# Optimization experiments

Hardware: AMD Instinct MI355X
Metric: run time of the kernel (lower is better)

Reference implementation:

```python
import jax, jax.numpy as jnp
import numpy as np

K = 8
NUM_BLOCKS = 4
ALPHA = K / (K + 1)  # 8/9


def _knn_norm_adj(xyz, k):
    """xyz: (B, 3, N) -> symmetric-normalized GCN adjacency (B, N, N).

    Mirrors knn_point(k, xyz, xyz) -> indices[:, 1:] -> get_adjacency_matrix,
    then the (input-independent) DenseGCNConv normalization: self loops set to 1,
    deg clamped >= 1, D^-1/2 A D^-1/2. adj is identical for every GCN call, so
    it is normalized once here.
    """
    x2 = jnp.sum(xyz * xyz, axis=1)                       # (B, N)
    inner = jnp.einsum('bci,bcj->bij', xyz, xyz)          # (B, N, N)
    dist = x2[:, :, None] + x2[:, None, :] - 2.0 * inner  # squared pairwise dist
    _, idx = jax.lax.top_k(-dist, k)                      # (B, N, k); self (dist 0) first
    nbr = idx[:, :, 1:]                                   # drop self -> k-1 neighbors
    B, N = x2.shape
    adj = jnp.zeros((B, N, N), xyz.dtype)
    adj = adj.at[jnp.arange(B)[:, None, None],
                 jnp.arange(N)[None, :, None], nbr].set(1.0)
    ar = jnp.arange(N)
    adj = adj.at[:, ar, ar].set(1.0)                      # add_loop=True
    dis = jnp.clip(jnp.sum(adj, axis=-1), 1.0, None) ** -0.5  # (B, N)
    return dis[:, :, None] * adj * dis[:, None, :]


def setup_inputs() -> dict:
    key = jax.random.key(0)
    ks = jax.random.split(key, 6)
    B, N, C = 16, 2048, 128
    s = 1.0 / np.sqrt(C).astype(np.float32)
    return {
        'xyz': jax.random.normal(ks[0], (B, 3, N), jnp.float32),
        'points': jax.random.normal(ks[1], (B, C, N), jnp.float32),
        'Wc': jax.random.normal(ks[2], (4, C, C), jnp.float32) * s,   # nn.Linear weights (out,in)
        'Wg': jax.random.normal(ks[3], (4, C, C), jnp.float32) * s,   # DenseGCNConv lin weights
        'Wuc': jax.random.normal(ks[4], (6, C), jnp.float32) * s,
        'Wug': jax.random.normal(ks[5], (6, C), jnp.float32) * s,
    }


def reference(xyz, points, Wc, Wg, Wuc, Wug):
    adj = _knn_norm_adj(xyz, K)                 # (B, N, N)
    pts = jnp.swapaxes(points, 1, 2)            # (B, N, C) channel-last internally
    for i in range(NUM_BLOCKS):
        shortcut = pts
        act = jax.nn.relu(pts)
        center = jnp.einsum('bnc,dc->bnd', act, Wc[i])                 # Linear on relu(points)
        grouped = adj @ jnp.einsum('bnc,dc->bnd', shortcut, Wg[i])     # DenseGCNConv on shortcut
        pts = (1.0 - ALPHA) * grouped + ALPHA * center + shortcut
    # unpool head
    points_xyz = jnp.einsum('bnd,od->bno', pts, Wuc)                   # (B, N, 6)
    grouped_xyz = adj @ jnp.einsum('bnd,od->bno', pts, Wug)            # (B, N, 6)
    new = ALPHA * points_xyz + (1.0 - ALPHA) * grouped_xyz
    B, N, _ = new.shape
    new = jnp.swapaxes(new, 1, 2).reshape(B, 3, 2, N) + xyz[:, :, None, :]
    new_xyz = new.reshape(B, 3, 2 * N)
    return new_xyz, jnp.swapaxes(pts, 1, 2)     # ((B,3,2N), (B,C,N))
```

## Files before the change

kernel.cpp:

```cpp
#include <hip/hip_runtime.h>
#include <hip/hip_bf16.h>

static constexpr int NB = 16;
static constexpr int NP = 2048;
static constexpr int NC = 128;
#define ALPHA_F ((float)(8.0/9.0))
#define OMA_F   ((float)(1.0 - 8.0/9.0))

typedef __attribute__((ext_vector_type(8))) short bfrag;
typedef __attribute__((ext_vector_type(4))) float ffrag;

union BU { bfrag v; uint4 u; unsigned int w[4]; };

__device__ inline void split2(float x, float y, unsigned& hi, unsigned& lo) {
    __hip_bfloat162 h = __float22bfloat162_rn(make_float2(x, y));
    float2 hb = __bfloat1622float2(h);
    __hip_bfloat162 l = __float22bfloat162_rn(make_float2(x - hb.x, y - hb.y));
    __builtin_memcpy(&hi, &h, 4);
    __builtin_memcpy(&lo, &l, 4);
}

__device__ inline void split1(float x, unsigned short& h, unsigned short& l) {
    __hip_bfloat16 hb = __float2bfloat16(x);
    float hf = __bfloat162float(hb);
    __hip_bfloat16 lb = __float2bfloat16(x - hf);
    __builtin_memcpy(&h, &hb, 2);
    __builtin_memcpy(&l, &lb, 2);
}

__global__ __launch_bounds__(256) void knn_kernel(const float* __restrict__ xyz,
                                                  int* __restrict__ nbr) {
    __shared__ float4 sp[NP];
    __shared__ float  md[64][33];
    __shared__ int    mi[64][33];
    int b = blockIdx.y;
    const float* X = xyz + (size_t)b * 3 * NP;
    for (int m = threadIdx.x; m < NP; m += 256) {
        float x = X[m], y = X[NP + m], z = X[2 * NP + m];
        sp[m ^ ((m >> 5) & 7)] = make_float4(x, y, z, x * x + y * y + z * z);
    }
    __syncthreads();

    int tid = threadIdx.x;
    int p = tid >> 2;
    int q = tid & 3;
    int base = blockIdx.x * 64;
    int n = base + p;
    float4 me = sp[n ^ ((n >> 5) & 7)];
    float xi = me.x, yi = me.y, zi = me.z, qi = me.w;

    unsigned gd[8];
#pragma unroll
    for (int t = 0; t < 8; ++t) gd[t] = 0x7F7FFFFFu;
#pragma unroll 1
    for (int gg = 0; gg < 16; ++gg) {
        int g = q * 16 + gg;
        const float4* gp = sp + g * 32;
        float m0 = 3.4e38f, m1 = m0, m2 = m0, m3 = m0;
#pragma unroll
        for (int k = 0; k < 32; k += 4) {
            float4 a0 = gp[(k + 0) ^ q];
            float4 a1 = gp[(k + 1) ^ q];
            float4 a2 = gp[(k + 2) ^ q];
            float4 a3 = gp[(k + 3) ^ q];
            m0 = fminf(m0, qi + a0.w - 2.0f * (xi * a0.x + yi * a0.y + zi * a0.z));
            m1 = fminf(m1, qi + a1.w - 2.0f * (xi * a1.x + yi * a1.y + zi * a1.z));
            m2 = fminf(m2, qi + a2.w - 2.0f * (xi * a2.x + yi * a2.y + zi * a2.z));
            m3 = fminf(m3, qi + a3.w - 2.0f * (xi * a3.x + yi * a3.y + zi * a3.z));
        }
        float gm = fmaxf(fminf(fminf(m0, m1), fminf(m2, m3)), 0.0f);
        unsigned pg; __builtin_memcpy(&pg, &gm, 4);
        pg = (pg & ~63u) | (unsigned)g;
        unsigned prev = gd[0];
        gd[0] = gd[0] < pg ? gd[0] : pg;
#pragma unroll
        for (int t = 1; t < 8; ++t) {
            unsigned mx = prev > pg ? prev : pg;
            prev = gd[t];
            gd[t] = gd[t] < mx ? gd[t] : mx;
        }
    }

#define CEU(A, B) { unsigned _lo = (A) < (B) ? (A) : (B); \
                    unsigned _hi = (A) < (B) ? (B) : (A); (A) = _lo; (B) = _hi; }
    unsigned cA[8];
#pragma unroll
    for (int i = 0; i < 8; ++i) {
        unsigned pb = (unsigned)__shfl_xor((int)gd[7 - i], 1);
        cA[i] = gd[i] < pb ? gd[i] : pb;
    }
    CEU(cA[0], cA[4]); CEU(cA[1], cA[5]); CEU(cA[2], cA[6]); CEU(cA[3], cA[7]);
    CEU(cA[0], cA[2]); CEU(cA[1], cA[3]); CEU(cA[4], cA[6]); CEU(cA[5], cA[7]);
    CEU(cA[0], cA[1]); CEU(cA[2], cA[3]); CEU(cA[4], cA[5]); CEU(cA[6], cA[7]);
    unsigned dA[8];
#pragma unroll
    for (int i = 0; i < 8; ++i) {
        unsigned pb = (unsigned)__shfl_xor((int)cA[7 - i], 2);
        dA[i] = cA[i] < pb ? cA[i] : pb;
    }
    unsigned long long mask = 0ull;
#pragma unroll
    for (int i = 0; i < 8; ++i) mask |= (1ull << (dA[i] & 63u));

    float bd[8]; int bi[8];
#pragma unroll
    for (int t = 0; t < 8; ++t) { bd[t] = 3.4e38f; bi[t] = 0; }
    while (mask) {
        int g = (int)__builtin_ctzll(mask);
        mask &= (mask - 1ull);
        int sw = g & 7;
        int jb = g * 32 + q;
#pragma unroll
        for (int i = 0; i < 8; ++i) {
            int j0 = jb + i * 4;
            float4 c4v = sp[j0 ^ sw];
            float inner = xi * c4v.x + yi * c4v.y + zi * c4v.z;
            float d = qi + c4v.w - 2.0f * inner;
            bool c[8];
#pragma unroll
            for (int t = 0; t < 8; ++t) c[t] = d < bd[t];
#pragma unroll
            for (int t = 7; t >= 1; --t) {
                bd[t] = c[t - 1] ? bd[t - 1] : (c[t] ? d : bd[t]);
                bi[t] = c[t - 1] ? bi[t - 1] : (c[t] ? j0 : bi[t]);
            }
            bd[0] = c[0] ? d : bd[0];
            bi[0] = c[0] ? j0 : bi[0];
        }
    }
#pragma unroll
    for (int t = 0; t < 8; ++t) {
        md[p][q * 8 + t] = bd[t];
        mi[p][q * 8 + t] = bi[t];
    }
    __syncthreads();

    if (tid < 64) {
        float fd[8]; int fi[8];
#pragma unroll
        for (int t = 0; t < 8; ++t) { fd[t] = 3.4e38f; fi[t] = 0; }
#pragma unroll 4
        for (int cc = 0; cc < 32; ++cc) {
            float d = md[tid][cc];
            int j = mi[tid][cc];
            bool c[8];
#pragma unroll
            for (int t = 0; t < 8; ++t) c[t] = d < fd[t];
#pragma unroll
            for (int t = 7; t >= 1; --t) {
                fd[t] = c[t - 1] ? fd[t - 1] : (c[t] ? d : fd[t]);
                fi[t] = c[t - 1] ? fi[t - 1] : (c[t] ? j : fi[t]);
            }
            fd[0] = c[0] ? d : fd[0];
            fi[0] = c[0] ? j : fi[0];
        }
        int row = b * NP + base + tid;
#pragma unroll
        for (int t = 0; t < 7; ++t) nbr[row * 7 + t] = fi[t + 1];
    }
}

__global__ __launch_bounds__(256) void transpose_kernel(const float* __restrict__ in,
                                                        float* __restrict__ out,
                                                        int R, int S) {
    __shared__ float t[32][33];
    int b = blockIdx.z;
    int s0 = blockIdx.x * 32, r0 = blockIdx.y * 32;
    const float* I = in + (size_t)b * R * S;
    float* O = out + (size_t)b * R * S;
#pragma unroll
    for (int i = 0; i < 4; ++i) {
        int r = r0 + threadIdx.y + i * 8;
        t[threadIdx.y + i * 8][threadIdx.x] = I[(size_t)r * S + s0 + threadIdx.x];
    }
    __syncthreads();
#pragma unroll
    for (int i = 0; i < 4; ++i) {
        int s = s0 + threadIdx.y + i * 8;
        O[(size_t)s * R + r0 + threadIdx.x] = t[threadIdx.x][threadIdx.y + i * 8];
    }
}

__global__ __launch_bounds__(256) void prep_w_kernel(const float* __restrict__ Wc,
                                                     const float* __restrict__ Wg,
                                                     uint4* __restrict__ WP) {
    int t = blockIdx.x * 256 + threadIdx.x;
    int ncol = t & 127;
    int quad = (t >> 7) & 3;
    int s = (t >> 9) & 3;
    int mat = (t >> 11) & 1;
    int layer = t >> 12;
    const float* W = (mat ? Wg : Wc) + (size_t)layer * NC * NC + (size_t)ncol * NC + s * 32 + quad * 8;
    float4 a = *((const float4*)W);
    float4 b = *((const float4*)(W + 4));
    BU hi, lo;
    split2(a.x, a.y, hi.w[0], lo.w[0]);
    split2(a.z, a.w, hi.w[1], lo.w[1]);
    split2(b.x, b.y, hi.w[2], lo.w[2]);
    split2(b.z, b.w, hi.w[3], lo.w[3]);
    WP[t * 2] = hi.u;
    WP[t * 2 + 1] = lo.u;
}

template <int MODE>
__global__ __launch_bounds__(512) void gemm_fused_kernel(const float* __restrict__ Asrc,
                                                         const float* __restrict__ Y2in,
                                                         const int* __restrict__ nbr,
                                                         const uint4* __restrict__ WPc,
                                                         const uint4* __restrict__ WPg,
                                                         float* __restrict__ Zout,
                                                         float* __restrict__ Y2out) {
    __shared__ unsigned short AhT[64][136];
    __shared__ unsigned short AlT[64][136];
    __shared__ int s_nb[448];
    int tid = threadIdx.x;
    int wid = tid >> 6, lane = tid & 63;
    int quad = lane >> 4, l15 = lane & 15;
    int xcd = blockIdx.x & 7;
    int slot = blockIdx.x >> 3;
    int bb = xcd * 2 + (slot >> 5);
    int n0 = (slot & 31) << 6;
    size_t m0 = (size_t)bb * NP + n0;
    int ncol = wid * 16 + l15;

    BU Bch[4], Bcl[4], Bgh[4], Bgl[4];
#pragma unroll
    for (int s = 0; s < 4; ++s) {
        int idx = ((s * 4 + quad) * 128 + ncol) * 2;
        Bch[s].u = WPc[idx];
        Bcl[s].u = WPc[idx + 1];
        Bgh[s].u = WPg[idx];
        Bgl[s].u = WPg[idx + 1];
    }

    if (MODE == 1) {
        if (tid < 448) s_nb[tid] = nbr[m0 * 7 + tid];
        __syncthreads();
        size_t bbase = (size_t)bb * NP;
#pragma unroll 1
        for (int it = 0; it < 4; ++it) {
            int f = tid + it * 512;
            int r = f >> 5, c4 = (f & 31) * 4;
            size_t row = m0 + r;
            float4 z = *((const float4*)(Asrc + row * NC + c4));
            float4 acc = *((const float4*)(Y2in + row * NC + c4));
#pragma unroll
            for (int t = 0; t < 7; ++t) {
                int j = s_nb[r * 7 + t];
                float4 v = *((const float4*)(Y2in + (bbase + (size_t)j) * NC + c4));
                acc.x += v.x; acc.y += v.y; acc.z += v.z; acc.w += v.w;
            }
            float4 a;
            a.x = OMA_F * (0.125f * acc.x) + z.x;
            a.y = OMA_F * (0.125f * acc.y) + z.y;
            a.z = OMA_F * (0.125f * acc.z) + z.z;
            a.w = OMA_F * (0.125f * acc.w) + z.w;
            unsigned h01, l01, h23, l23;
            split2(a.x, a.y, h01, l01);
            split2(a.z, a.w, h23, l23);
            *((uint2*)&AhT[r][c4]) = make_uint2(h01, h23);
            *((uint2*)&AlT[r][c4]) = make_uint2(l01, l23);
        }
    } else {
#pragma unroll
        for (int it = 0; it < 4; ++it) {
            int f = tid + it * 512;
            int c = f >> 4, rq = (f & 15) * 4;
            float4 v = *((const float4*)(Asrc + ((size_t)bb * NC + c) * NP + n0 + rq));
            float vv[4] = {v.x, v.y, v.z, v.w};
#pragma unroll
            for (int k = 0; k < 4; ++k) {
                unsigned short h, l;
                split1(vv[k], h, l);
                AhT[rq + k][c] = h;
                AlT[rq + k][c] = l;
            }
        }
    }
    __syncthreads();

    ffrag accC[4], accG[4];
#pragma unroll
    for (int mt = 0; mt < 4; ++mt) { accC[mt] = (ffrag)0.0f; accG[mt] = (ffrag)0.0f; }

#pragma unroll
    for (int s = 0; s < 4; ++s) {
#pragma unroll
        for (int mt = 0; mt < 4; ++mt) {
            int m = mt * 16 + l15;
            int k = s * 32 + quad * 8;
            BU ah, al, rh, rl;
            ah.u = *((const uint4*)&AhT[m][k]);
            al.u = *((const uint4*)&AlT[m][k]);
#pragma unroll
            for (int w = 0; w < 4; ++w) {
                unsigned msk = ((ah.w[w] & 0x80008000u) >> 15) * 0xFFFFu;
                rh.w[w] = ah.w[w] & ~msk;
                rl.w[w] = al.w[w] & ~msk;
            }
            accC[mt] = __builtin_amdgcn_mfma_f32_16x16x32_bf16(rh.v, Bch[s].v, accC[mt], 0, 0, 0);
            accC[mt] = __builtin_amdgcn_mfma_f32_16x16x32_bf16(rh.v, Bcl[s].v, accC[mt], 0, 0, 0);
            accC[mt] = __builtin_amdgcn_mfma_f32_16x16x32_bf16(rl.v, Bch[s].v, accC[mt], 0, 0, 0);
            accG[mt] = __builtin_amdgcn_mfma_f32_16x16x32_bf16(ah.v, Bgh[s].v, accG[mt], 0, 0, 0);
            accG[mt] = __builtin_amdgcn_mfma_f32_16x16x32_bf16(ah.v, Bgl[s].v, accG[mt], 0, 0, 0);
            accG[mt] = __builtin_amdgcn_mfma_f32_16x16x32_bf16(al.v, Bgh[s].v, accG[mt], 0, 0, 0);
        }
    }

#pragma unroll
    for (int mt = 0; mt < 4; ++mt) {
        int rbase = mt * 16 + quad * 4;
#pragma unroll
        for (int r = 0; r < 4; ++r) {
            int rr = rbase + r;
            unsigned hb = ((unsigned)AhT[rr][ncol]) << 16;
            unsigned lb = ((unsigned)AlT[rr][ncol]) << 16;
            float hp, lp;
            __builtin_memcpy(&hp, &hb, 4);
            __builtin_memcpy(&lp, &lb, 4);
            float p = hp + lp;
            size_t idx = (m0 + rr) * NC + ncol;
            Zout[idx] = p + ALPHA_F * accC[mt][r];
            Y2out[idx] = accG[mt][r];
        }
    }
}

__global__ __launch_bounds__(256) void agg_kernel(const float* __restrict__ Z,
                                                  const float* __restrict__ Y2,
                                                  const int* __restrict__ nbr,
                                                  float* __restrict__ Pout) {
    int tid = threadIdx.x;
    int lane = tid & 31, rl = tid >> 5;
    int xcd = blockIdx.x & 7;
    int slot = blockIdx.x >> 3;
    int bb = xcd * 2 + (slot >> 8);
    int rblk = slot & 255;
    size_t row = ((size_t)bb << 11) + rblk * 8 + rl;
    const int* nb = nbr + row * 7;
    size_t off = row * NC + lane * 4;
    float4 ys = *((const float4*)(Y2 + off));
    size_t bbase = (size_t)bb * NP * NC;
#pragma unroll
    for (int t = 0; t < 7; ++t) {
        int j = nb[t];
        float4 v = *((const float4*)(Y2 + bbase + (size_t)j * NC + lane * 4));
        ys.x += v.x; ys.y += v.y; ys.z += v.z; ys.w += v.w;
    }
    float4 z = *((const float4*)(Z + off));
    float4 o;
    o.x = OMA_F * (0.125f * ys.x) + z.x;
    o.y = OMA_F * (0.125f * ys.y) + z.y;
    o.z = OMA_F * (0.125f * ys.z) + z.z;
    o.w = OMA_F * (0.125f * ys.w) + z.w;
    *((float4*)(Pout + off)) = o;
}

__global__ __launch_bounds__(256) void final_gemm_kernel(const float* __restrict__ P,
                                                         const float* __restrict__ Wuc,
                                                         const float* __restrict__ Wug,
                                                         float* __restrict__ U) {
    __shared__ float s1[6 * NC], s2[6 * NC];
    for (int m = threadIdx.x; m < 6 * NC; m += 256) { s1[m] = Wuc[m]; s2[m] = Wug[m]; }
    __syncthreads();
    size_t row = (size_t)blockIdx.x * 256 + threadIdx.x;
    const float4* prow = (const float4*)(P + row * NC);
    float a1[6] = {0, 0, 0, 0, 0, 0}, a2[6] = {0, 0, 0, 0, 0, 0};
#pragma unroll 4
    for (int c4 = 0; c4 < NC / 4; ++c4) {
        float4 p = prow[c4];
#pragma unroll
        for (int o = 0; o < 6; ++o) {
            float4 w1 = *((const float4*)&s1[o * NC + c4 * 4]);
            float4 w2 = *((const float4*)&s2[o * NC + c4 * 4]);
            a1[o] += p.x * w1.x + p.y * w1.y + p.z * w1.z + p.w * w1.w;
            a2[o] += p.x * w2.x + p.y * w2.y + p.z * w2.z + p.w * w2.w;
        }
    }
#pragma unroll
    for (int o = 0; o < 6; ++o) {
        U[row * 12 + o] = a1[o];
        U[row * 12 + 6 + o] = a2[o];
    }
}

__global__ __launch_bounds__(256) void final_out_kernel(const float* __restrict__ U,
                                                        const int* __restrict__ nbr,
                                                        const float* __restrict__ xyz,
                                                        float* __restrict__ out) {
    size_t row = (size_t)blockIdx.x * 256 + threadIdx.x;
    int b = (int)(row >> 11), n = (int)(row & 2047);
    const int* nb = nbr + row * 7;
    float u1[6], u2[6];
#pragma unroll
    for (int o = 0; o < 6; ++o) { u1[o] = U[row * 12 + o]; u2[o] = U[row * 12 + 6 + o]; }
#pragma unroll
    for (int t = 0; t < 7; ++t) {
        int j = nb[t];
        const float* Uj = U + ((size_t)b * NP + j) * 12 + 6;
#pragma unroll
        for (int o = 0; o < 6; ++o) u2[o] += Uj[o];
    }
#pragma unroll
    for (int c = 0; c < 3; ++c)
#pragma unroll
        for (int s = 0; s < 2; ++s) {
            int o = c * 2 + s;
            float val = ALPHA_F * u1[o] + OMA_F * (0.125f * u2[o])
                      + xyz[(size_t)b * 3 * NP + (size_t)c * NP + n];
            out[(size_t)b * 3 * 2 * NP + (size_t)c * 2 * NP + (size_t)s * NP + n] = val;
        }
}

extern "C" void kernel_launch(void* const* d_in, const int* in_sizes, int n_in,
                              void* d_out, int out_size, void* d_ws, size_t ws_size,
                              hipStream_t stream) {
    const float* xyz    = (const float*)d_in[0];
    const float* points = (const float*)d_in[1];
    const float* Wc     = (const float*)d_in[2];
    const float* Wg     = (const float*)d_in[3];
    const float* Wuc    = (const float*)d_in[4];
    const float* Wug    = (const float*)d_in[5];
    float* out = (float*)d_out;

    char* ws = (char*)d_ws;
    size_t o = 0;
    int* nbr  = (int*)(ws + o);     o += (size_t)NB * NP * 7 * 4;
    uint4* WP = (uint4*)(ws + o);   o += (size_t)32768 * 16;
    float* Za = (float*)(ws + o);   o += (size_t)NB * NP * NC * 4;
    float* Ya = (float*)(ws + o);   o += (size_t)NB * NP * NC * 4;
    float* Zb = (float*)(ws + o);   o += (size_t)NB * NP * NC * 4;
    float* Yb = (float*)(ws + o);   o += (size_t)NB * NP * NC * 4;
    float* U  = (float*)(ws + o);   o += (size_t)NB * NP * 12 * 4;

    const int GEMM_GRID = NB * NP / 64;
    #define WPC(L) (WP + (size_t)((L) * 2 + 0) * 4096)
    #define WPG(L) (WP + (size_t)((L) * 2 + 1) * 4096)

    prep_w_kernel<<<64, 256, 0, stream>>>(Wc, Wg, WP);
    knn_kernel<<<dim3(NP / 64, NB), 256, 0, stream>>>(xyz, nbr);
    gemm_fused_kernel<0><<<GEMM_GRID, 512, 0, stream>>>(points, nullptr, nullptr,
        WPC(0), WPG(0), Za, Ya);
    gemm_fused_kernel<1><<<GEMM_GRID, 512, 0, stream>>>(Za, Ya, nbr,
        WPC(1), WPG(1), Zb, Yb);
    gemm_fused_kernel<1><<<GEMM_GRID, 512, 0, stream>>>(Zb, Yb, nbr,
        WPC(2), WPG(2), Za, Ya);
    gemm_fused_kernel<1><<<GEMM_GRID, 512, 0, stream>>>(Za, Ya, nbr,
        WPC(3), WPG(3), Zb, Yb);
    float* P5 = Za;
    agg_kernel<<<dim3(NB * NP / 8), 256, 0, stream>>>(Zb, Yb, nbr, P5);
    final_gemm_kernel<<<dim3(NB * NP / 256), 256, 0, stream>>>(P5, Wuc, Wug, U);
    final_out_kernel<<<dim3(NB * NP / 256), 256, 0, stream>>>(U, nbr, xyz, out);
    transpose_kernel<<<dim3(NC / 32, NP / 32, NB), dim3(32, 8), 0, stream>>>(
        P5, out + (size_t)NB * 3 * 2 * NP, NP, NC);
}
```

Measured before the change: 217.9 us.

## Fuse final aggregation, unpool projection and output transpose into one kernel

Merges the last aggregation kernel, the 6-output unpool GEMM and the channel-first transpose into a single agg2 kernel. Each warp computes the aggregated row, reduces its dot products with Wuc/Wug through wave shuffles, and writes the transposed tile to the output through shared memory. This drops the P5 intermediate round trip through global memory and two kernel launches. The cost is extra shared memory and shuffle reductions per block, plus narrow 8-element strided output writes.

```diff
diff --git a/kernel.cpp b/kernel.cpp
--- a/kernel.cpp
+++ b/kernel.cpp
@@ -157,27 +157,6 @@
         int row = b * NP + base + tid;
 #pragma unroll
         for (int t = 0; t < 7; ++t) nbr[row * 7 + t] = fi[t + 1];
-    }
-}
-
-__global__ __launch_bounds__(256) void transpose_kernel(const float* __restrict__ in,
-                                                        float* __restrict__ out,
-                                                        int R, int S) {
-    __shared__ float t[32][33];
-    int b = blockIdx.z;
-    int s0 = blockIdx.x * 32, r0 = blockIdx.y * 32;
-    const float* I = in + (size_t)b * R * S;
-    float* O = out + (size_t)b * R * S;
-#pragma unroll
-    for (int i = 0; i < 4; ++i) {
-        int r = r0 + threadIdx.y + i * 8;
-        t[threadIdx.y + i * 8][threadIdx.x] = I[(size_t)r * S + s0 + threadIdx.x];
-    }
-    __syncthreads();
-#pragma unroll
-    for (int i = 0; i < 4; ++i) {
-        int s = s0 + threadIdx.y + i * 8;
-        O[(size_t)s * R + r0 + threadIdx.x] = t[threadIdx.x][threadIdx.y + i * 8];
     }
 }
 
@@ -326,17 +305,25 @@
     }
 }
 
-__global__ __launch_bounds__(256) void agg_kernel(const float* __restrict__ Z,
-                                                  const float* __restrict__ Y2,
-                                                  const int* __restrict__ nbr,
-                                                  float* __restrict__ Pout) {
+__global__ __launch_bounds__(256) void agg2_kernel(const float* __restrict__ Z,
+                                                   const float* __restrict__ Y2,
+                                                   const int* __restrict__ nbr,
+                                                   const float* __restrict__ Wuc,
+                                                   const float* __restrict__ Wug,
+                                                   float* __restrict__ U,
+                                                   float* __restrict__ out2) {
+    __shared__ float s1[6 * NC], s2[6 * NC];
+    __shared__ float sm[8][132];
     int tid = threadIdx.x;
     int lane = tid & 31, rl = tid >> 5;
+    for (int m = tid; m < 6 * NC; m += 256) { s1[m] = Wuc[m]; s2[m] = Wug[m]; }
+
     int xcd = blockIdx.x & 7;
     int slot = blockIdx.x >> 3;
     int bb = xcd * 2 + (slot >> 8);
     int rblk = slot & 255;
-    size_t row = ((size_t)bb << 11) + rblk * 8 + rl;
+    int n0 = rblk * 8;
+    size_t row = ((size_t)bb << 11) + n0 + rl;
     const int* nb = nbr + row * 7;
     size_t off = row * NC + lane * 4;
     float4 ys = *((const float4*)(Y2 + off));
@@ -353,35 +340,44 @@
     o.y = OMA_F * (0.125f * ys.y) + z.y;
     o.z = OMA_F * (0.125f * ys.z) + z.z;
     o.w = OMA_F * (0.125f * ys.w) + z.w;
-    *((float4*)(Pout + off)) = o;
-}
-
-__global__ __launch_bounds__(256) void final_gemm_kernel(const float* __restrict__ P,
-                                                         const float* __restrict__ Wuc,
-                                                         const float* __restrict__ Wug,
-                                                         float* __restrict__ U) {
-    __shared__ float s1[6 * NC], s2[6 * NC];
-    for (int m = threadIdx.x; m < 6 * NC; m += 256) { s1[m] = Wuc[m]; s2[m] = Wug[m]; }
+
     __syncthreads();
-    size_t row = (size_t)blockIdx.x * 256 + threadIdx.x;
-    const float4* prow = (const float4*)(P + row * NC);
-    float a1[6] = {0, 0, 0, 0, 0, 0}, a2[6] = {0, 0, 0, 0, 0, 0};
-#pragma unroll 4
-    for (int c4 = 0; c4 < NC / 4; ++c4) {
-        float4 p = prow[c4];
-#pragma unroll
-        for (int o = 0; o < 6; ++o) {
-            float4 w1 = *((const float4*)&s1[o * NC + c4 * 4]);
-            float4 w2 = *((const float4*)&s2[o * NC + c4 * 4]);
-            a1[o] += p.x * w1.x + p.y * w1.y + p.z * w1.z + p.w * w1.w;
-            a2[o] += p.x * w2.x + p.y * w2.y + p.z * w2.z + p.w * w2.w;
-        }
-    }
-#pragma unroll
-    for (int o = 0; o < 6; ++o) {
-        U[row * 12 + o] = a1[o];
-        U[row * 12 + 6 + o] = a2[o];
-    }
+    *((float4*)&sm[rl][lane * 4]) = o;
+
+    float a1[6], a2[6];
+#pragma unroll
+    for (int oo = 0; oo < 6; ++oo) {
+        float4 w1 = *((const float4*)&s1[oo * NC + lane * 4]);
+        float4 w2 = *((const float4*)&s2[oo * NC + lane * 4]);
+        a1[oo] = o.x * w1.x + o.y * w1.y + o.z * w1.z + o.w * w1.w;
+        a2[oo] = o.x * w2.x + o.y * w2.y + o.z * w2.z + o.w * w2.w;
+    }
+#pragma unroll
+    for (int s = 1; s < 32; s <<= 1) {
+#pragma unroll
+        for (int oo = 0; oo < 6; ++oo) {
+            a1[oo] += __shfl_xor(a1[oo], s);
+            a2[oo] += __shfl_xor(a2[oo], s);
+        }
+    }
+    if (lane == 0) {
+        float* Ur = U + row * 12;
+        float4 u0 = make_float4(a1[0], a1[1], a1[2], a1[3]);
+        float4 u1 = make_float4(a1[4], a1[5], a2[0], a2[1]);
+        float4 u2 = make_float4(a2[2], a2[3], a2[4], a2[5]);
+        *((float4*)(Ur + 0)) = u0;
+        *((float4*)(Ur + 4)) = u1;
+        *((float4*)(Ur + 8)) = u2;
+    }
+
+    __syncthreads();
+    int c = tid >> 1, h = tid & 1;
+    float4 v;
+    v.x = sm[4 * h + 0][c];
+    v.y = sm[4 * h + 1][c];
+    v.z = sm[4 * h + 2][c];
+    v.w = sm[4 * h + 3][c];
+    *((float4*)(out2 + ((size_t)bb * NC + c) * NP + n0 + 4 * h)) = v;
 }
 
 __global__ __launch_bounds__(256) void final_out_kernel(const float* __restrict__ U,
@@ -447,10 +443,7 @@
         WPC(2), WPG(2), Za, Ya);
     gemm_fused_kernel<1><<<GEMM_GRID, 512, 0, stream>>>(Za, Ya, nbr,
         WPC(3), WPG(3), Zb, Yb);
-    float* P5 = Za;
-    agg_kernel<<<dim3(NB * NP / 8), 256, 0, stream>>>(Zb, Yb, nbr, P5);
-    final_gemm_kernel<<<dim3(NB * NP / 256), 256, 0, stream>>>(P5, Wuc, Wug, U);
+    float* out2 = out + (size_t)NB * 3 * 2 * NP;
+    agg2_kernel<<<dim3(NB * NP / 8), 256, 0, stream>>>(Zb, Yb, nbr, Wuc, Wug, U, out2);
     final_out_kernel<<<dim3(NB * NP / 256), 256, 0, stream>>>(U, nbr, xyz, out);
-    transpose_kernel<<<dim3(NC / 32, NP / 32, NB), dim3(32, 8), 0, stream>>>(
-        P5, out + (size_t)NB * 3 * 2 * NP, NP, NC);
-}
+}
```

Result: faster. 208.0 us (-4.5%).
